# Optimization experiments

Measured on AMD Instinct MI355X. Metric: run time of the kernel, lower is better.

The kernel has to match this reference:

```python
import jax, jax.numpy as jnp
import numpy as np

N = 50000      # num_labels (nodes)
HID = 64       # hidden_dim
HEADS = 4
CH = 16        # hidden_dim // 4 per head
R = 4          # relations
E = 200000     # edges per relation
DEPTH = 2
SLOPE = 0.2    # GATv2 leaky_relu negative slope
EPS = 1e-5     # LayerNorm eps


def layer_norm(x, g, b):
    mu = jnp.mean(x, axis=-1, keepdims=True)
    var = jnp.mean((x - mu) ** 2, axis=-1, keepdims=True)
    return (x - mu) / jnp.sqrt(var + EPS) * g + b


def setup_inputs() -> dict:
    key = jax.random.key(0)
    ks = jax.random.split(key, 8)
    # edges with src != dst (PyG remove_self_loops is then a no-op)
    src = jax.random.randint(ks[0], (R, E), 0, N, dtype=jnp.int32)
    off = jax.random.randint(ks[1], (R, E), 1, N, dtype=jnp.int32)
    dst = ((src + off) % N).astype(jnp.int32)
    edge_index = jnp.stack([src, dst], axis=1)  # [R, 2, E]
    s = 1.0 / np.sqrt(HID)
    return {
        "label_embeddings": jax.random.normal(ks[2], (N, HID), jnp.float32) * 0.5,
        "entry_w": jax.random.normal(ks[3], (HID, HID), jnp.float32) * s,
        "entry_b": jnp.zeros((HID,), jnp.float32),
        "entry_ln_g": jnp.ones((HID,), jnp.float32),
        "entry_ln_b": jnp.zeros((HID,), jnp.float32),
        "conv_wl": jax.random.normal(ks[4], (DEPTH, R, HID, HEADS * CH), jnp.float32) * s,
        "conv_wr": jax.random.normal(ks[5], (DEPTH, R, HID, HEADS * CH), jnp.float32) * s,
        "conv_att": jax.random.normal(ks[6], (DEPTH, R, HEADS, CH), jnp.float32) * (1.0 / np.sqrt(CH)),
        "conv_bias": jnp.zeros((DEPTH, R, HEADS * CH), jnp.float32),
        "norm_g": jnp.ones((HID,), jnp.float32),
        "norm_b": jnp.zeros((HID,), jnp.float32),
        "edge_index": edge_index,
    }


def _gatv2_layer(x, wl, wr, att, bias, src, dst):
    """One GATv2Conv over one relation. x:[N,HID]; returns [N, HEADS*CH]."""
    xl = (x @ wl).reshape(N, HEADS, CH)  # source transform
    xr = (x @ wr).reshape(N, HEADS, CH)  # target transform
    m = xl[src] + xr[dst]                          # [E+N, HEADS, CH]
    e = jnp.einsum('ehc,hc->eh', jax.nn.leaky_relu(m, SLOPE), att)  # [E+N, HEADS]
    # segment softmax over incoming edges of each dst node
    emax = jax.ops.segment_max(e, dst, num_segments=N)  # [N, HEADS]
    a = jnp.exp(e - emax[dst])
    denom = jax.ops.segment_sum(a, dst, num_segments=N)
    alpha = a / denom[dst]                          # every node has a self-loop -> denom > 0
    msg = xl[src] * alpha[..., None]                # [E+N, HEADS, CH]
    out = jax.ops.segment_sum(msg, dst, num_segments=N).reshape(N, HEADS * CH)
    return out + bias


def reference(label_embeddings, entry_w, entry_b, entry_ln_g, entry_ln_b,
              conv_wl, conv_wr, conv_att, conv_bias, norm_g, norm_b, edge_index):
    x = jax.nn.gelu(layer_norm(label_embeddings @ entry_w + entry_b, entry_ln_g, entry_ln_b),
                    approximate=False)
    loop = jnp.arange(N, dtype=edge_index.dtype)
    for layer in range(DEPTH):
        outs = []
        for r in range(R):
            src = jnp.concatenate([edge_index[r, 0], loop])  # add self-loops (PyG default)
            dst = jnp.concatenate([edge_index[r, 1], loop])
            outs.append(_gatv2_layer(x, conv_wl[layer, r], conv_wr[layer, r],
                                     conv_att[layer, r], conv_bias[layer, r], src, dst))
        x = sum(outs) / R                              # HeteroConv aggr='mean'
        x = layer_norm(jax.nn.gelu(x, approximate=False), norm_g, norm_b)  # dropout = identity (eval)
    return x
```

## Files before the change

### kernel.cpp

```cpp
#include <hip/hip_runtime.h>
#include <hip/hip_bf16.h>

#define NN 50000
#define RR 4
#define EE 200000
#define CAP 32

typedef __hip_bfloat16 bf16;
typedef __attribute__((ext_vector_type(8))) short short8;
typedef __attribute__((ext_vector_type(4))) float float4v;
typedef __attribute__((ext_vector_type(2))) float float2v;

__device__ __forceinline__ float b2f(bf16 v) { return __bfloat162float(v); }
__device__ __forceinline__ unsigned short f2bu(float v) {
    bf16 h = __float2bfloat16(v);
    return *(unsigned short*)&h;
}
__device__ __forceinline__ float ldf(const void* p, int i, int isbf) {
    return isbf ? __bfloat162float(((const bf16*)p)[i]) : ((const float*)p)[i];
}
__device__ __forceinline__ int dtype_isbf(const void* lg) {
    return ((const unsigned*)lg)[0] == 0x3F803F80u;
}
__device__ __forceinline__ float gelu_exact(float x) {
    return 0.5f * x * (1.0f + erff(x * 0.70710678118654752f));
}
__device__ __forceinline__ float lrelu(float m) { return fmaxf(m, 0.2f * m); }
__device__ __forceinline__ float2v bp2(unsigned u) {
    float2v f;
    f.x = __uint_as_float(u << 16);
    f.y = __uint_as_float(u & 0xffff0000u);
    return f;
}
__device__ __forceinline__ float2v lrelu2(float2v m) {
    float2v s = m * 0.2f;
    float2v r;
    r.x = fmaxf(m.x, s.x);
    r.y = fmaxf(m.y, s.y);
    return r;
}

#define PW_ENTRY_W 0
#define PW_ENTRY_B 4096
#define PW_LN_G    4160
#define PW_LN_B    4224
#define PW_WL      4288
#define PW_ATT     69824
#define PW_BIAS    70336
#define PW_NG      70848
#define PW_NB      70912
#define PW_TOT     70976

#define WT_ELEMS (2 * RR * 128 * 64)

__global__ __launch_bounds__(256) void cvt_k(const void* ew, const void* eb, const void* lg,
                                             const void* lb, const void* wl, const void* wr,
                                             const void* at, const void* bi, const void* ng,
                                             const void* nb,
                                             float* __restrict__ P, bf16* __restrict__ WT,
                                             int* __restrict__ cnt) {
    int i = blockIdx.x * 256 + threadIdx.x;
    int isbf = dtype_isbf(lg);
    if (i < RR * NN) cnt[i] = 0;
    if (i < WT_ELEMS) {
        int k = i & 63;
        int c = (i >> 6) & 127;
        int lr = i >> 13;
        float v = (c < 64) ? ldf(wl, (lr * 64 + k) * 64 + c, isbf)
                           : ldf(wr, (lr * 64 + k) * 64 + (c - 64), isbf);
        WT[i] = __float2bfloat16(v);
    }
    if (i < PW_TOT) {
        const void* src = nullptr;
        int off = 0;
        if (i < PW_ENTRY_B)      { src = ew; off = i - PW_ENTRY_W; }
        else if (i < PW_LN_G)    { src = eb; off = i - PW_ENTRY_B; }
        else if (i < PW_LN_B)    { src = lg; off = i - PW_LN_G; }
        else if (i < PW_WL)      { src = lb; off = i - PW_LN_B; }
        else if (i < PW_ATT)     { src = nullptr; }
        else if (i < PW_BIAS)    { src = at; off = i - PW_ATT; }
        else if (i < PW_NG)      { src = bi; off = i - PW_BIAS; }
        else if (i < PW_NB)      { src = ng; off = i - PW_NG; }
        else                     { src = nb; off = i - PW_NB; }
        if (src) P[i] = ldf(src, off, isbf);
    }
}

__global__ void scatter_k(const int* __restrict__ ei, int* __restrict__ cnt,
                          int* __restrict__ col) {
    int e = blockIdx.x * 256 + threadIdx.x;
    int r = blockIdx.y;
    if (e < EE) {
        int s = ei[r * 2 * EE + e];
        int d = ei[r * 2 * EE + EE + e];
        int p = atomicAdd(&cnt[r * NN + d], 1);
        if (p < CAP) col[((size_t)r * NN + d) * CAP + p] = s;
    }
}

__global__ __launch_bounds__(256) void entry_k(const void* __restrict__ emb,
                                               const void* __restrict__ lg,
                                               const float* __restrict__ P,
                                               bf16* __restrict__ xout) {
    int wave = (blockIdx.x * 256 + threadIdx.x) >> 6;
    int c = threadIdx.x & 63;
    if (wave >= NN) return;
    int isbf = dtype_isbf(lg);
    float ev = ldf(emb, wave * 64 + c, isbf);
    float acc = 0.f;
#pragma unroll 8
    for (int k = 0; k < 64; k++) {
        float xv = __shfl(ev, k, 64);
        acc += xv * P[PW_ENTRY_W + k * 64 + c];
    }
    acc += P[PW_ENTRY_B + c];
    float s = acc;
#pragma unroll
    for (int m = 1; m < 64; m <<= 1) s += __shfl_xor(s, m, 64);
    float mu = s * (1.f / 64.f);
    float d = acc - mu;
    float vs = d * d;
#pragma unroll
    for (int m = 1; m < 64; m <<= 1) vs += __shfl_xor(vs, m, 64);
    float var = vs * (1.f / 64.f);
    float y = d * rsqrtf(var + 1e-5f) * P[PW_LN_G + c] + P[PW_LN_B + c];
    xout[wave * 64 + c] = __float2bfloat16(gelu_exact(y));
}

__global__ __launch_bounds__(256) void gemm_m(const bf16* __restrict__ X,
                                              const bf16* __restrict__ WTlayer,
                                              bf16* __restrict__ xlB,
                                              bf16* __restrict__ xrB) {
    int r = blockIdx.y;
    const short* Xs = (const short*)X;
    const short* WT = (const short*)(WTlayer + (size_t)r * 8192);
    bf16* xl = xlB + (size_t)r * NN * 64;
    bf16* xr = xrB + (size_t)r * NN * 64;

    __shared__ float sh[16 * 132];
    int t = threadIdx.x;
    int w = t >> 6;
    int lane = t & 63;
    int m = lane & 15, kq = lane >> 4;
    int row0 = blockIdx.x * 16;

    const short* ap = Xs + (row0 + m) * 64 + kq * 8;
    short8 a0 = *(const short8*)ap;
    short8 a1 = *(const short8*)(ap + 32);

#pragma unroll
    for (int tile = 0; tile < 2; tile++) {
        int ct = w * 2 + tile;
        int c0 = ct * 16 + m;
        const short* bp = WT + c0 * 64 + kq * 8;
        short8 b0 = *(const short8*)bp;
        short8 b1 = *(const short8*)(bp + 32);
        float4v acc = {0.f, 0.f, 0.f, 0.f};
        asm volatile(
            "v_mfma_f32_16x16x32_bf16 %0, %1, %2, %0\n\t"
            "v_mfma_f32_16x16x32_bf16 %0, %3, %4, %0\n\t"
            "s_nop 7\n\t"
            "s_nop 7"
            : "+v"(acc)
            : "v"(a0), "v"(b0), "v"(a1), "v"(b1));
#pragma unroll
        for (int i = 0; i < 4; i++) sh[(kq * 4 + i) * 132 + c0] = acc[i];
    }
    __syncthreads();
    int row = t >> 4, cg = (t & 15) * 8;
    float v0 = sh[row * 132 + cg + 0], v1 = sh[row * 132 + cg + 1];
    float v2 = sh[row * 132 + cg + 2], v3 = sh[row * 132 + cg + 3];
    float v4 = sh[row * 132 + cg + 4], v5 = sh[row * 132 + cg + 5];
    float v6 = sh[row * 132 + cg + 6], v7 = sh[row * 132 + cg + 7];
    uint4 u;
    u.x = ((unsigned)f2bu(v1) << 16) | f2bu(v0);
    u.y = ((unsigned)f2bu(v3) << 16) | f2bu(v2);
    u.z = ((unsigned)f2bu(v5) << 16) | f2bu(v4);
    u.w = ((unsigned)f2bu(v7) << 16) | f2bu(v6);
    size_t grow = row0 + row;
    if (cg < 64) *(uint4*)&xl[grow * 64 + cg] = u;
    else         *(uint4*)&xr[grow * 64 + (cg - 64)] = u;
}

__global__ __launch_bounds__(256) void aggfin_k(const bf16* __restrict__ xlB,
                                                const bf16* __restrict__ xrB,
                                                const float* __restrict__ attL,
                                                const float* __restrict__ biasL,
                                                const int* __restrict__ cnt,
                                                const int* __restrict__ col,
                                                const float* __restrict__ P,
                                                const void* __restrict__ lg,
                                                void* __restrict__ outp,
                                                int finalOut) {
    __shared__ float shRes[RR][4][68];
    int t = threadIdx.x;
    int r = t >> 6;
    int lane = t & 63;
    int nodeBase = blockIdx.x * 4;
    int nn = lane >> 4, es = (lane >> 2) & 3, h = lane & 3;
    int node = nodeBase + nn;

    const unsigned* xl = (const unsigned*)(xlB + (size_t)r * NN * 64);
    const unsigned* xr = (const unsigned*)(xrB + (size_t)r * NN * 64);
    const float* att = attL + r * 64;
    const float* bias = biasL + r * 64;

    float2v at2[8], xr2[8];
    {
        const float4* ap = (const float4*)(att + h * 16);
#pragma unroll
        for (int i = 0; i < 4; i++) {
            float4 a = ap[i];
            at2[2 * i].x = a.x * 1.44269504f; at2[2 * i].y = a.y * 1.44269504f;
            at2[2 * i + 1].x = a.z * 1.44269504f; at2[2 * i + 1].y = a.w * 1.44269504f;
        }
        const uint4* q = (const uint4*)(xr + node * 32 + h * 8);
        uint4 u0 = q[0], u1 = q[1];
        xr2[0] = bp2(u0.x); xr2[1] = bp2(u0.y); xr2[2] = bp2(u0.z); xr2[3] = bp2(u0.w);
        xr2[4] = bp2(u1.x); xr2[5] = bp2(u1.y); xr2[6] = bp2(u1.z); xr2[7] = bp2(u1.w);
    }
    int cn = cnt[r * NN + node];
    if (cn > CAP) cn = CAP;
    int total = cn + 1;
    int kmax = total;
    kmax = max(kmax, __shfl_xor(kmax, 16, 64));
    kmax = max(kmax, __shfl_xor(kmax, 32, 64));
    const int* bucket = col + ((size_t)r * NN + node) * CAP;

    float2v A2[8];
#pragma unroll
    for (int i = 0; i < 8; i++) A2[i] = (float2v){0.f, 0.f};
    float D = 0.f;

    int k = es;
    if (k < kmax) {
        bool act = k < total;
        int src = (act && k > 0) ? bucket[k - 1] : node;
        const uint4* q = (const uint4*)(xl + src * 32 + h * 8);
        uint4 u0 = q[0], u1 = q[1];
        for (;;) {
            int kn = k + 4;
            bool more = kn < kmax;
            bool actn = false;
            uint4 n0, n1;
            if (more) {
                actn = kn < total;
                int srcn = actn ? bucket[kn - 1] : node;
                const uint4* qn = (const uint4*)(xl + srcn * 32 + h * 8);
                n0 = qn[0]; n1 = qn[1];
            }
            float2v x2[8];
            x2[0] = bp2(u0.x); x2[1] = bp2(u0.y); x2[2] = bp2(u0.z); x2[3] = bp2(u0.w);
            x2[4] = bp2(u1.x); x2[5] = bp2(u1.y); x2[6] = bp2(u1.z); x2[7] = bp2(u1.w);
            float2v t2 = (float2v){0.f, 0.f};
#pragma unroll
            for (int i = 0; i < 8; i++)
                t2 = t2 + lrelu2(x2[i] + xr2[i]) * at2[i];
            float tt = t2.x + t2.y;
            float p = act ? exp2f(tt) : 0.f;
            D += p;
            float2v p2 = (float2v){p, p};
#pragma unroll
            for (int i = 0; i < 8; i++) A2[i] = A2[i] + p2 * x2[i];
            if (!more) break;
            k = kn; act = actn; u0 = n0; u1 = n1;
        }
    }
    D += __shfl_xor(D, 4, 64);
    D += __shfl_xor(D, 8, 64);
#pragma unroll
    for (int i = 0; i < 8; i++) {
        A2[i].x += __shfl_xor(A2[i].x, 4, 64);
        A2[i].x += __shfl_xor(A2[i].x, 8, 64);
        A2[i].y += __shfl_xor(A2[i].y, 4, 64);
        A2[i].y += __shfl_xor(A2[i].y, 8, 64);
    }
    if (es == 0) {
        float inv = __builtin_amdgcn_rcpf(D);
        const float4* bp = (const float4*)(bias + h * 16);
        float* dst = &shRes[r][nn][h * 16];
#pragma unroll
        for (int i = 0; i < 4; i++) {
            float4 b = bp[i];
            dst[4 * i + 0] = A2[2 * i].x * inv + b.x;
            dst[4 * i + 1] = A2[2 * i].y * inv + b.y;
            dst[4 * i + 2] = A2[2 * i + 1].x * inv + b.z;
            dst[4 * i + 3] = A2[2 * i + 1].y * inv + b.w;
        }
    }
    __syncthreads();
    int wn = t >> 6, c = t & 63;
    float v = shRes[0][wn][c] + shRes[1][wn][c] + shRes[2][wn][c] + shRes[3][wn][c];
    v = gelu_exact(v * 0.25f);
    float s = v;
#pragma unroll
    for (int m = 1; m < 64; m <<= 1) s += __shfl_xor(s, m, 64);
    float mu = s * (1.f / 64.f);
    float d = v - mu;
    float vs = d * d;
#pragma unroll
    for (int m = 1; m < 64; m <<= 1) vs += __shfl_xor(vs, m, 64);
    float var = vs * (1.f / 64.f);
    float y = d * rsqrtf(var + 1e-5f) * P[PW_NG + c] + P[PW_NB + c];
    size_t o = (size_t)(nodeBase + wn) * 64 + c;
    if (!finalOut) {
        ((bf16*)outp)[o] = __float2bfloat16(y);
    } else {
        if (dtype_isbf(lg)) ((bf16*)outp)[o] = __float2bfloat16(y);
        else                ((float*)outp)[o] = y;
    }
}

extern "C" void kernel_launch(void* const* d_in, const int* in_sizes, int n_in,
                              void* d_out, int out_size, void* d_ws, size_t ws_size,
                              hipStream_t stream) {
    const void* emb = d_in[0];
    const void* lg  = d_in[3];
    const int*  ei  = (const int*)d_in[11];

    const size_t BUF = (size_t)NN * 64;

    bf16* X   = (bf16*)d_ws;
    bf16* XL  = X + BUF;
    bf16* XR  = XL + RR * BUF;
    bf16* WT  = XR + RR * BUF;
    float* P  = (float*)(WT + WT_ELEMS);
    int* cnt  = (int*)(P + PW_TOT);
    int* col  = cnt + RR * NN;

    int cvtN = RR * NN;
    cvt_k<<<(cvtN + 255) / 256, 256, 0, stream>>>(d_in[1], d_in[2], d_in[3], d_in[4],
                                                  d_in[5], d_in[6], d_in[7], d_in[8],
                                                  d_in[9], d_in[10], P, WT, cnt);
    scatter_k<<<dim3((EE + 255) / 256, RR), 256, 0, stream>>>(ei, cnt, col);

    int nodeBlocks = (NN + 3) / 4;
    int tileBlocks = NN / 16;

    entry_k<<<nodeBlocks, 256, 0, stream>>>(emb, lg, P, X);

    for (int l = 0; l < 2; l++) {
        gemm_m<<<dim3(tileBlocks, RR), 256, 0, stream>>>(X, WT + (size_t)l * RR * 8192, XL, XR);
        aggfin_k<<<nodeBlocks, 256, 0, stream>>>(
            XL, XR, P + PW_ATT + (size_t)l * RR * 64, P + PW_BIAS + (size_t)l * RR * 64,
            cnt, col, P, lg, (l == 0) ? (void*)X : d_out, l);
    }
}
```

Baseline: 368.0 us.

## Process multiple row tiles per GEMM block and front-load edge gathers in aggregation

The GEMM kernel now handles 80 rows per block, loading the weight fragments once and prefetching the next 16-row A tile while the current one is computed and stored. This amortises the weight loads and launch cost across five tiles. The aggregation kernel issues the count, the first two bucket indices and their xl row gathers up front, before the attention setup. It then runs the first two edges unconditionally with clamped source indices, so the initial memory latency overlaps with setup work. The cost is more live registers, reads of bucket slots that may be unused, and an extra barrier per GEMM tile.

Result: faster. 324.0 us (-12.0%).

```diff
diff --git a/kernel.cpp b/kernel.cpp
--- a/kernel.cpp
+++ b/kernel.cpp
@@ -127,6 +127,7 @@
     xout[wave * 64 + c] = __float2bfloat16(gelu_exact(y));
 }
 
+#define GR 80
 __global__ __launch_bounds__(256) void gemm_m(const bf16* __restrict__ X,
                                               const bf16* __restrict__ WTlayer,
                                               bf16* __restrict__ xlB,
@@ -142,44 +143,81 @@
     int w = t >> 6;
     int lane = t & 63;
     int m = lane & 15, kq = lane >> 4;
-    int row0 = blockIdx.x * 16;
+    int row0 = blockIdx.x * GR;
+
+    short8 b0[2], b1[2];
+    int c0t[2];
+#pragma unroll
+    for (int tile = 0; tile < 2; tile++) {
+        int ct = w * 2 + tile;
+        int c0 = ct * 16 + m;
+        c0t[tile] = c0;
+        const short* bp = WT + c0 * 64 + kq * 8;
+        b0[tile] = *(const short8*)bp;
+        b1[tile] = *(const short8*)(bp + 32);
+    }
 
     const short* ap = Xs + (row0 + m) * 64 + kq * 8;
     short8 a0 = *(const short8*)ap;
     short8 a1 = *(const short8*)(ap + 32);
 
-#pragma unroll
-    for (int tile = 0; tile < 2; tile++) {
-        int ct = w * 2 + tile;
-        int c0 = ct * 16 + m;
-        const short* bp = WT + c0 * 64 + kq * 8;
-        short8 b0 = *(const short8*)bp;
-        short8 b1 = *(const short8*)(bp + 32);
-        float4v acc = {0.f, 0.f, 0.f, 0.f};
-        asm volatile(
-            "v_mfma_f32_16x16x32_bf16 %0, %1, %2, %0\n\t"
-            "v_mfma_f32_16x16x32_bf16 %0, %3, %4, %0\n\t"
-            "s_nop 7\n\t"
-            "s_nop 7"
-            : "+v"(acc)
-            : "v"(a0), "v"(b0), "v"(a1), "v"(b1));
-#pragma unroll
-        for (int i = 0; i < 4; i++) sh[(kq * 4 + i) * 132 + c0] = acc[i];
-    }
-    __syncthreads();
-    int row = t >> 4, cg = (t & 15) * 8;
-    float v0 = sh[row * 132 + cg + 0], v1 = sh[row * 132 + cg + 1];
-    float v2 = sh[row * 132 + cg + 2], v3 = sh[row * 132 + cg + 3];
-    float v4 = sh[row * 132 + cg + 4], v5 = sh[row * 132 + cg + 5];
-    float v6 = sh[row * 132 + cg + 6], v7 = sh[row * 132 + cg + 7];
-    uint4 u;
-    u.x = ((unsigned)f2bu(v1) << 16) | f2bu(v0);
-    u.y = ((unsigned)f2bu(v3) << 16) | f2bu(v2);
-    u.z = ((unsigned)f2bu(v5) << 16) | f2bu(v4);
-    u.w = ((unsigned)f2bu(v7) << 16) | f2bu(v6);
-    size_t grow = row0 + row;
-    if (cg < 64) *(uint4*)&xl[grow * 64 + cg] = u;
-    else         *(uint4*)&xr[grow * 64 + (cg - 64)] = u;
+    for (int g = 0; g < 5; g++) {
+        short8 na0, na1;
+        if (g < 4) {
+            const short* np = ap + (g + 1) * 16 * 64;
+            na0 = *(const short8*)np;
+            na1 = *(const short8*)(np + 32);
+        }
+#pragma unroll
+        for (int tile = 0; tile < 2; tile++) {
+            float4v acc = {0.f, 0.f, 0.f, 0.f};
+            asm volatile(
+                "v_mfma_f32_16x16x32_bf16 %0, %1, %2, %0\n\t"
+                "v_mfma_f32_16x16x32_bf16 %0, %3, %4, %0\n\t"
+                "s_nop 7\n\t"
+                "s_nop 7"
+                : "+v"(acc)
+                : "v"(a0), "v"(b0[tile]), "v"(a1), "v"(b1[tile]));
+#pragma unroll
+            for (int i = 0; i < 4; i++) sh[(kq * 4 + i) * 132 + c0t[tile]] = acc[i];
+        }
+        __syncthreads();
+        {
+            int row = t >> 4, cg = (t & 15) * 8;
+            float v0 = sh[row * 132 + cg + 0], v1 = sh[row * 132 + cg + 1];
+            float v2 = sh[row * 132 + cg + 2], v3 = sh[row * 132 + cg + 3];
+            float v4 = sh[row * 132 + cg + 4], v5 = sh[row * 132 + cg + 5];
+            float v6 = sh[row * 132 + cg + 6], v7 = sh[row * 132 + cg + 7];
+            uint4 u;
+            u.x = ((unsigned)f2bu(v1) << 16) | f2bu(v0);
+            u.y = ((unsigned)f2bu(v3) << 16) | f2bu(v2);
+            u.z = ((unsigned)f2bu(v5) << 16) | f2bu(v4);
+            u.w = ((unsigned)f2bu(v7) << 16) | f2bu(v6);
+            size_t grow = row0 + g * 16 + row;
+            if (cg < 64) *(uint4*)&xl[grow * 64 + cg] = u;
+            else         *(uint4*)&xr[grow * 64 + (cg - 64)] = u;
+        }
+        __syncthreads();
+        a0 = na0; a1 = na1;
+    }
+}
+
+__device__ __forceinline__ void edge_accum(uint4 u0, uint4 u1, bool act,
+                                           const float2v at2[8], const float2v xr2[8],
+                                           float2v A2[8], float& D) {
+    float2v x2[8];
+    x2[0] = bp2(u0.x); x2[1] = bp2(u0.y); x2[2] = bp2(u0.z); x2[3] = bp2(u0.w);
+    x2[4] = bp2(u1.x); x2[5] = bp2(u1.y); x2[6] = bp2(u1.z); x2[7] = bp2(u1.w);
+    float2v t2 = (float2v){0.f, 0.f};
+#pragma unroll
+    for (int i = 0; i < 8; i++)
+        t2 = t2 + lrelu2(x2[i] + xr2[i]) * at2[i];
+    float tt = t2.x + t2.y;
+    float p = act ? exp2f(tt) : 0.f;
+    D += p;
+    float2v p2 = (float2v){p, p};
+#pragma unroll
+    for (int i = 0; i < 8; i++) A2[i] = A2[i] + p2 * x2[i];
 }
 
 __global__ __launch_bounds__(256) void aggfin_k(const bf16* __restrict__ xlB,
@@ -204,68 +242,55 @@
     const unsigned* xr = (const unsigned*)(xrB + (size_t)r * NN * 64);
     const float* att = attL + r * 64;
     const float* bias = biasL + r * 64;
+    const int* bucket = col + ((size_t)r * NN + node) * CAP;
+
+    int cn_raw = cnt[r * NN + node];
+    int c0raw = (es > 0) ? bucket[es - 1] : node;
+    int c1raw = bucket[es + 3];
+    const uint4* qr = (const uint4*)(xr + (size_t)node * 32 + h * 8);
+    uint4 r0 = qr[0], r1 = qr[1];
+
+    unsigned s0 = (unsigned)c0raw < (unsigned)NN ? (unsigned)c0raw : (unsigned)(NN - 1);
+    unsigned s1 = (unsigned)c1raw < (unsigned)NN ? (unsigned)c1raw : (unsigned)(NN - 1);
+    const uint4* q0 = (const uint4*)(xl + (size_t)s0 * 32 + h * 8);
+    uint4 u0 = q0[0], u1 = q0[1];
+    const uint4* q1 = (const uint4*)(xl + (size_t)s1 * 32 + h * 8);
+    uint4 w0 = q1[0], w1 = q1[1];
 
     float2v at2[8], xr2[8];
     {
-        const float4* ap = (const float4*)(att + h * 16);
+        const float4* apv = (const float4*)(att + h * 16);
 #pragma unroll
         for (int i = 0; i < 4; i++) {
-            float4 a = ap[i];
+            float4 a = apv[i];
             at2[2 * i].x = a.x * 1.44269504f; at2[2 * i].y = a.y * 1.44269504f;
             at2[2 * i + 1].x = a.z * 1.44269504f; at2[2 * i + 1].y = a.w * 1.44269504f;
         }
-        const uint4* q = (const uint4*)(xr + node * 32 + h * 8);
-        uint4 u0 = q[0], u1 = q[1];
-        xr2[0] = bp2(u0.x); xr2[1] = bp2(u0.y); xr2[2] = bp2(u0.z); xr2[3] = bp2(u0.w);
-        xr2[4] = bp2(u1.x); xr2[5] = bp2(u1.y); xr2[6] = bp2(u1.z); xr2[7] = bp2(u1.w);
-    }
-    int cn = cnt[r * NN + node];
-    if (cn > CAP) cn = CAP;
+        xr2[0] = bp2(r0.x); xr2[1] = bp2(r0.y); xr2[2] = bp2(r0.z); xr2[3] = bp2(r0.w);
+        xr2[4] = bp2(r1.x); xr2[5] = bp2(r1.y); xr2[6] = bp2(r1.z); xr2[7] = bp2(r1.w);
+    }
+    int cn = cn_raw > CAP ? CAP : cn_raw;
     int total = cn + 1;
     int kmax = total;
     kmax = max(kmax, __shfl_xor(kmax, 16, 64));
     kmax = max(kmax, __shfl_xor(kmax, 32, 64));
-    const int* bucket = col + ((size_t)r * NN + node) * CAP;
 
     float2v A2[8];
 #pragma unroll
     for (int i = 0; i < 8; i++) A2[i] = (float2v){0.f, 0.f};
     float D = 0.f;
 
-    int k = es;
-    if (k < kmax) {
+    edge_accum(u0, u1, es < total, at2, xr2, A2, D);
+    edge_accum(w0, w1, es + 4 < total, at2, xr2, A2, D);
+
+    for (int k = es + 8; k < kmax; k += 4) {
         bool act = k < total;
-        int src = (act && k > 0) ? bucket[k - 1] : node;
-        const uint4* q = (const uint4*)(xl + src * 32 + h * 8);
-        uint4 u0 = q[0], u1 = q[1];
-        for (;;) {
-            int kn = k + 4;
-            bool more = kn < kmax;
-            bool actn = false;
-            uint4 n0, n1;
-            if (more) {
-                actn = kn < total;
-                int srcn = actn ? bucket[kn - 1] : node;
-                const uint4* qn = (const uint4*)(xl + srcn * 32 + h * 8);
-                n0 = qn[0]; n1 = qn[1];
-            }
-            float2v x2[8];
-            x2[0] = bp2(u0.x); x2[1] = bp2(u0.y); x2[2] = bp2(u0.z); x2[3] = bp2(u0.w);
-            x2[4] = bp2(u1.x); x2[5] = bp2(u1.y); x2[6] = bp2(u1.z); x2[7] = bp2(u1.w);
-            float2v t2 = (float2v){0.f, 0.f};
-#pragma unroll
-            for (int i = 0; i < 8; i++)
-                t2 = t2 + lrelu2(x2[i] + xr2[i]) * at2[i];
-            float tt = t2.x + t2.y;
-            float p = act ? exp2f(tt) : 0.f;
-            D += p;
-            float2v p2 = (float2v){p, p};
-#pragma unroll
-            for (int i = 0; i < 8; i++) A2[i] = A2[i] + p2 * x2[i];
-            if (!more) break;
-            k = kn; act = actn; u0 = n0; u1 = n1;
-        }
-    }
+        int sr = act ? bucket[k - 1] : node;
+        const uint4* q = (const uint4*)(xl + (size_t)sr * 32 + h * 8);
+        uint4 t0 = q[0], t1 = q[1];
+        edge_accum(t0, t1, act, at2, xr2, A2, D);
+    }
+
     D += __shfl_xor(D, 4, 64);
     D += __shfl_xor(D, 8, 64);
 #pragma unroll
@@ -335,12 +360,12 @@
     scatter_k<<<dim3((EE + 255) / 256, RR), 256, 0, stream>>>(ei, cnt, col);
 
     int nodeBlocks = (NN + 3) / 4;
-    int tileBlocks = NN / 16;
+    int gemmBlocks = NN / GR;
 
     entry_k<<<nodeBlocks, 256, 0, stream>>>(emb, lg, P, X);
 
     for (int l = 0; l < 2; l++) {
-        gemm_m<<<dim3(tileBlocks, RR), 256, 0, stream>>>(X, WT + (size_t)l * RR * 8192, XL, XR);
+        gemm_m<<<dim3(gemmBlocks, RR), 256, 0, stream>>>(X, WT + (size_t)l * RR * 8192, XL, XR);
         aggfin_k<<<nodeBlocks, 256, 0, stream>>>(
             XL, XR, P + PW_ATT + (size_t)l * RR * 64, P + PW_BIAS + (size_t)l * RR * 64,
             cnt, col, P, lg, (l == 0) ? (void*)X : d_out, l);
```
